# Kernel tuning notes

Hardware: AMD Instinct MI355X
Metric: run time of the kernel (lower is better)

The kernel has to match this reference:

```python
import jax, jax.numpy as jnp
import numpy as np

N_HEADS = 16
EMBED_DIM = 1024
HEAD_DIM = EMBED_DIM // N_HEADS
B, S = 4, 2048


def setup_inputs() -> dict:
    key = jax.random.key(0)
    k1, k2, k3, k4 = jax.random.split(key, 4)
    scale = 1.0 / np.sqrt(EMBED_DIM)
    x = jax.random.normal(k1, (B, S, EMBED_DIM), dtype=jnp.float32)
    Wq = jax.random.normal(k2, (EMBED_DIM, EMBED_DIM), dtype=jnp.float32) * scale
    Wk = jax.random.normal(k3, (EMBED_DIM, EMBED_DIM), dtype=jnp.float32) * scale
    Wv = jax.random.normal(k4, (EMBED_DIM, EMBED_DIM), dtype=jnp.float32) * scale
    return {"x": x, "Wq": Wq, "Wk": Wk, "Wv": Wv}


def reference(x, Wq, Wk, Wv):
    b, s, d = x.shape
    # torch nn.Linear(bias=False): y = x @ W.T
    def proj(W):
        return (x @ W.T).reshape(b, s, N_HEADS, HEAD_DIM).transpose(0, 2, 1, 3)  # [b,h,s,hd]
    q, k, v = proj(Wq), proj(Wk), proj(Wv)
    # scores scaled by sqrt(embed_dim) as in the source (not head_dim)
    scores = jnp.einsum('bhqd,bhkd->bhqk', q, k) / jnp.sqrt(jnp.float32(d))
    attn = jax.nn.softmax(scores, axis=-1)
    out = jnp.einsum('bhqk,bhkd->bhqd', attn, v)  # [b,h,s,hd]
    return out.transpose(0, 2, 1, 3).reshape(b, s, d)
```

## Files before the change

kernel.cpp:

```cpp
#include <hip/hip_runtime.h>

#define S_LEN  2048
#define NHEAD  16
#define HDIM   64
#define DMODEL 1024
#define XN     (4 * 2048 * 1024)
#define WN     (1024 * 1024)

typedef float  floatx4 __attribute__((ext_vector_type(4)));
typedef __bf16 bf16x8  __attribute__((ext_vector_type(8)));
typedef __bf16 bf16x4  __attribute__((ext_vector_type(4)));
typedef unsigned int u32;

union B8 {
  bf16x8 v8;
  bf16x4 v4[2];
  __bf16 e[8];
  uint4  u;
};

typedef __attribute__((address_space(1))) u32 gu32;
typedef __attribute__((address_space(3))) u32 lu32;
__device__ __forceinline__ void gld16(const void* g, void* l) {
  __builtin_amdgcn_global_load_lds((const gu32*)g, (lu32*)l, 16, 0, 0);
}

__global__ __launch_bounds__(256) void cvt_kernel(
    const float* __restrict__ x,  const float* __restrict__ Wq,
    const float* __restrict__ Wk, const float* __restrict__ Wv,
    __bf16* __restrict__ xb, __bf16* __restrict__ Wb)
{
  const size_t base = ((size_t)blockIdx.x * 256 + threadIdx.x) * 8;
  const float* src;
  __bf16* dst;
  float scl = 1.0f;
  if (base < XN) {
    src = x + base;
    dst = xb + base;
  } else {
    const size_t j = base - XN;
    const int mat = (int)(j >> 20);
    const size_t o = j & (WN - 1);
    src = (mat == 0 ? Wq : mat == 1 ? Wk : Wv) + o;
    dst = Wb + ((size_t)mat << 20) + o;
    if (mat == 0) scl = 0.045084220027780106f;
  }
  float4 a = *(const float4*)src;
  float4 b = *(const float4*)(src + 4);
  B8 r;
  r.e[0] = (__bf16)(a.x * scl); r.e[1] = (__bf16)(a.y * scl);
  r.e[2] = (__bf16)(a.z * scl); r.e[3] = (__bf16)(a.w * scl);
  r.e[4] = (__bf16)(b.x * scl); r.e[5] = (__bf16)(b.y * scl);
  r.e[6] = (__bf16)(b.z * scl); r.e[7] = (__bf16)(b.w * scl);
  *(bf16x8*)dst = r.v8;
}

__global__ __launch_bounds__(256) void proj_kernel(
    const __bf16* __restrict__ xb, const __bf16* __restrict__ Wb,
    __bf16* __restrict__ Qo, __bf16* __restrict__ Ko, __bf16* __restrict__ Vt)
{
  __shared__ __attribute__((aligned(16))) union {
    struct { __bf16 As[2][128 * 32]; __bf16 Bs[2][128 * 32]; } st;
    __bf16 Es[4][64][72];
  } sh;

  const int tid  = threadIdx.x;
  const int lane = tid & 63;
  const int wv   = tid >> 6;
  const int l15  = lane & 15;
  const int quad = lane >> 4;

  const int row0 = blockIdx.y * 128;
  const int n0   = blockIdx.x * 128;
  const int wrow = (wv >> 1) * 64;
  const int wcol = (wv & 1) * 64;

  floatx4 acc[4][4];
  #pragma unroll
  for (int i = 0; i < 4; i++)
    #pragma unroll
    for (int j = 0; j < 4; j++) acc[i][j] = (floatx4)0.0f;

  const int swz = quad ^ ((l15 >> 1) & 3);

  const int c0    = tid;
  const int r0_   = c0 >> 2;
  const int g0    = (c0 & 3) ^ ((c0 >> 3) & 3);
  const int c1    = tid + 256;
  const int r1_   = c1 >> 2;
  const int g1    = (c1 & 3) ^ ((c1 >> 3) & 3);
  const size_t l0 = (size_t)(wv * 64) * 8;
  const size_t l1 = (size_t)(wv * 64 + 256) * 8;

  {
    gld16(xb + (size_t)(row0 + r0_) * DMODEL + 0 + g0 * 8, sh.st.As[0] + l0);
    gld16(Wb + (size_t)(n0 + r0_) * DMODEL + 0 + g0 * 8, sh.st.Bs[0] + l0);
    gld16(xb + (size_t)(row0 + r1_) * DMODEL + 0 + g1 * 8, sh.st.As[0] + l1);
    gld16(Wb + (size_t)(n0 + r1_) * DMODEL + 0 + g1 * 8, sh.st.Bs[0] + l1);
  }

  int buf = 0;
  for (int kk = 0; kk < DMODEL; kk += 32) {
    __syncthreads();
    if (kk + 32 < DMODEL) {
      const int nb_ = buf ^ 1;
      const int k2  = kk + 32;
      gld16(xb + (size_t)(row0 + r0_) * DMODEL + k2 + g0 * 8, sh.st.As[nb_] + l0);
      gld16(Wb + (size_t)(n0 + r0_) * DMODEL + k2 + g0 * 8, sh.st.Bs[nb_] + l0);
      gld16(xb + (size_t)(row0 + r1_) * DMODEL + k2 + g1 * 8, sh.st.As[nb_] + l1);
      gld16(Wb + (size_t)(n0 + r1_) * DMODEL + k2 + g1 * 8, sh.st.Bs[nb_] + l1);
    }

    B8 af[4], bg[4];
    #pragma unroll
    for (int mb = 0; mb < 4; mb++)
      af[mb].u = *(const uint4*)(sh.st.As[buf] + (size_t)(wrow + mb * 16 + l15) * 32 + swz * 8);
    #pragma unroll
    for (int nb = 0; nb < 4; nb++)
      bg[nb].u = *(const uint4*)(sh.st.Bs[buf] + (size_t)(wcol + nb * 16 + l15) * 32 + swz * 8);

    #pragma unroll
    for (int mb = 0; mb < 4; mb++)
      #pragma unroll
      for (int nb = 0; nb < 4; nb++)
        acc[mb][nb] = __builtin_amdgcn_mfma_f32_16x16x32_bf16(
            af[mb].v8, bg[nb].v8, acc[mb][nb], 0, 0, 0);
    buf ^= 1;
  }

  const int mat   = n0 >> 10;
  const int bb    = (row0 + wrow) >> 11;
  const int sbase = (row0 + wrow) & 2047;
  const int hh    = ((n0 & 1023) + wcol) >> 6;
  __syncthreads();

  if (mat < 2) {
    #pragma unroll
    for (int mb = 0; mb < 4; mb++)
      #pragma unroll
      for (int rr = 0; rr < 4; rr++)
        #pragma unroll
        for (int nb = 0; nb < 4; nb++)
          sh.Es[wv][mb * 16 + quad * 4 + rr][nb * 16 + l15] =
              (__bf16)acc[mb][nb][rr];
    __bf16* Out = (mat == 0) ? Qo : Ko;
    const size_t obase = ((size_t)(bb * NHEAD + hh) * S_LEN + sbase) * HDIM;
    #pragma unroll
    for (int t = 0; t < 8; t++) {
      const int lin = t * 64 + lane;
      const int s = lin >> 3, g = lin & 7;
      *(uint4*)&Out[obase + (size_t)s * HDIM + g * 8] =
          *(const uint4*)&sh.Es[wv][s][g * 8];
    }
  } else {
    #pragma unroll
    for (int mb = 0; mb < 4; mb++)
      #pragma unroll
      for (int nb = 0; nb < 4; nb++) {
        bf16x4 pk = { (__bf16)acc[mb][nb][0], (__bf16)acc[mb][nb][1],
                      (__bf16)acc[mb][nb][2], (__bf16)acc[mb][nb][3] };
        const int col = 32 * (mb >> 1) + 16 * (quad >> 1) + 8 * (quad & 1) +
                        4 * (mb & 1);
        *(bf16x4*)&sh.Es[wv][nb * 16 + l15][col] = pk;
      }
    const size_t vbase = (size_t)(bb * NHEAD + hh) * HDIM * S_LEN;
    #pragma unroll
    for (int t = 0; t < 8; t++) {
      const int lin = t * 64 + lane;
      const int d = lin >> 3, g = lin & 7;
      *(uint4*)&Vt[vbase + (size_t)d * S_LEN + sbase + g * 8] =
          *(const uint4*)&sh.Es[wv][d][g * 8];
    }
  }
}

__global__ __launch_bounds__(256, 2) void attn_kernel(
    const __bf16* __restrict__ Q, const __bf16* __restrict__ K,
    const __bf16* __restrict__ Vt, float* __restrict__ out)
{
  __shared__ __attribute__((aligned(16))) __bf16 Ks[2][64 * 64];
  __shared__ __attribute__((aligned(16))) __bf16 Vs[2][64 * 64];

  const int tid  = threadIdx.x;
  const int lane = tid & 63;
  const int wv   = tid >> 6;
  const int l15  = lane & 15;
  const int quad = lane >> 4;

  const int bh = blockIdx.x;
  const int q0 = blockIdx.y * 256;
  const int b  = bh >> 4;
  const int h  = bh & 15;

  const __bf16* Qb = Q  + (size_t)bh * S_LEN * HDIM;
  const __bf16* Kb = K  + (size_t)bh * S_LEN * HDIM;
  const __bf16* Vb = Vt + (size_t)bh * HDIM * S_LEN;

  B8 aq[4][2];
  #pragma unroll
  for (int nb = 0; nb < 4; nb++)
    #pragma unroll
    for (int kc = 0; kc < 2; kc++)
      aq[nb][kc].u = *(const uint4*)
          &Qb[(size_t)(q0 + wv * 64 + nb * 16 + l15) * HDIM + kc * 32 + quad * 8];

  floatx4 o[4][4];
  float rs[4];
  #pragma unroll
  for (int mt = 0; mt < 4; mt++)
    #pragma unroll
    for (int nb = 0; nb < 4; nb++) o[mt][nb] = (floatx4)0.0f;
  #pragma unroll
  for (int nb = 0; nb < 4; nb++) rs[nb] = 0.0f;

  const int swz0 = quad ^ (l15 & 7);
  const int swz1 = (4 + quad) ^ (l15 & 7);

  const int rA  = tid >> 3;
  const int gA  = (tid & 7) ^ ((tid >> 3) & 7);
  const int rB  = (tid + 256) >> 3;
  const int gB  = ((tid + 256) & 7) ^ (((tid + 256) >> 3) & 7);
  const size_t lA = (size_t)(wv * 64) * 8;
  const size_t lB = (size_t)(wv * 64 + 256) * 8;

  {
    gld16(Kb + (size_t)rA * HDIM + gA * 8, Ks[0] + lA);
    gld16(Vb + (size_t)rA * S_LEN + gA * 8, Vs[0] + lA);
    gld16(Kb + (size_t)rB * HDIM + gB * 8, Ks[0] + lB);
    gld16(Vb + (size_t)rB * S_LEN + gB * 8, Vs[0] + lB);
  }

  int buf = 0;
  for (int kv0 = 0; kv0 < S_LEN; kv0 += 64) {
    __syncthreads();
    if (kv0 + 64 < S_LEN) {
      const int nbuf = buf ^ 1;
      const int kv1  = kv0 + 64;
      gld16(Kb + (size_t)(kv1 + rA) * HDIM + gA * 8, Ks[nbuf] + lA);
      gld16(Vb + (size_t)rA * S_LEN + kv1 + gA * 8, Vs[nbuf] + lA);
      gld16(Kb + (size_t)(kv1 + rB) * HDIM + gB * 8, Ks[nbuf] + lB);
      gld16(Vb + (size_t)rB * S_LEN + kv1 + gB * 8, Vs[nbuf] + lB);
    }

    floatx4 sa[4][4];
    #pragma unroll
    for (int t = 0; t < 4; t++)
      #pragma unroll
      for (int nb = 0; nb < 4; nb++) sa[t][nb] = (floatx4)0.0f;

    #pragma unroll
    for (int kc = 0; kc < 2; kc++) {
      const int sw = kc ? swz1 : swz0;
      B8 ak[4];
      #pragma unroll
      for (int t = 0; t < 4; t++)
        ak[t].u = *(const uint4*)(Ks[buf] + (size_t)(t * 16 + l15) * 64 + sw * 8);
      #pragma unroll
      for (int t = 0; t < 4; t++)
        #pragma unroll
        for (int nb = 0; nb < 4; nb++)
          sa[t][nb] = __builtin_amdgcn_mfma_f32_16x16x32_bf16(
              ak[t].v8, aq[nb][kc].v8, sa[t][nb], 0, 0, 0);
    }

    #pragma unroll
    for (int kc = 0; kc < 2; kc++) {
      const int sw = kc ? swz1 : swz0;
      B8 pf[4];
      #pragma unroll
      for (int nb = 0; nb < 4; nb++) {
        float e0 = __builtin_amdgcn_exp2f(sa[2 * kc][nb][0]);
        float e1 = __builtin_amdgcn_exp2f(sa[2 * kc][nb][1]);
        float e2 = __builtin_amdgcn_exp2f(sa[2 * kc][nb][2]);
        float e3 = __builtin_amdgcn_exp2f(sa[2 * kc][nb][3]);
        float e4 = __builtin_amdgcn_exp2f(sa[2 * kc + 1][nb][0]);
        float e5 = __builtin_amdgcn_exp2f(sa[2 * kc + 1][nb][1]);
        float e6 = __builtin_amdgcn_exp2f(sa[2 * kc + 1][nb][2]);
        float e7 = __builtin_amdgcn_exp2f(sa[2 * kc + 1][nb][3]);
        rs[nb] += ((e0 + e1) + (e2 + e3)) + ((e4 + e5) + (e6 + e7));
        pf[nb].e[0] = (__bf16)e0; pf[nb].e[1] = (__bf16)e1;
        pf[nb].e[2] = (__bf16)e2; pf[nb].e[3] = (__bf16)e3;
        pf[nb].e[4] = (__bf16)e4; pf[nb].e[5] = (__bf16)e5;
        pf[nb].e[6] = (__bf16)e6; pf[nb].e[7] = (__bf16)e7;
      }
      B8 av[4];
      #pragma unroll
      for (int mt = 0; mt < 4; mt++)
        av[mt].u = *(const uint4*)(Vs[buf] + (size_t)(mt * 16 + l15) * 64 + sw * 8);
      #pragma unroll
      for (int mt = 0; mt < 4; mt++)
        #pragma unroll
        for (int nb = 0; nb < 4; nb++)
          o[mt][nb] = __builtin_amdgcn_mfma_f32_16x16x32_bf16(
              av[mt].v8, pf[nb].v8, o[mt][nb], 0, 0, 0);
    }
    buf ^= 1;
  }

  #pragma unroll
  for (int nb = 0; nb < 4; nb++) {
    float v = rs[nb];
    v += __shfl_xor(v, 16);
    v += __shfl_xor(v, 32);
    const float inv = 1.0f / v;
    const int q = q0 + wv * 64 + nb * 16 + l15;
    #pragma unroll
    for (int mt = 0; mt < 4; mt++) {
      float4 w = { o[mt][nb][0] * inv, o[mt][nb][1] * inv,
                   o[mt][nb][2] * inv, o[mt][nb][3] * inv };
      *(float4*)&out[((size_t)(b * S_LEN + q)) * DMODEL + h * HDIM +
                     mt * 16 + quad * 4] = w;
    }
  }
}

extern "C" void kernel_launch(void* const* d_in, const int* in_sizes, int n_in,
                              void* d_out, int out_size, void* d_ws, size_t ws_size,
                              hipStream_t stream) {
  const float* x  = (const float*)d_in[0];
  const float* Wq = (const float*)d_in[1];
  const float* Wk = (const float*)d_in[2];
  const float* Wv = (const float*)d_in[3];
  float* out = (float*)d_out;

  __bf16* xb = (__bf16*)d_ws;
  __bf16* Wb = xb + XN;
  __bf16* Q  = Wb + 3 * (size_t)WN;
  __bf16* K  = Q + (size_t)XN;
  __bf16* Vt = K + (size_t)XN;

  dim3 b256(256);
  cvt_kernel<<<dim3((XN + 3 * WN) / (256 * 8)), b256, 0, stream>>>(
      x, Wq, Wk, Wv, xb, Wb);

  dim3 g1(24, 64);
  proj_kernel<<<g1, b256, 0, stream>>>(xb, Wb, Q, K, Vt);

  dim3 g2(64, 8);
  attn_kernel<<<g2, b256, 0, stream>>>(Q, K, Vt, out);
}
```

Baseline: 222.9 us.

## Halve attention query tile and drop K/V double buffering for higher occupancy

The attention kernel now gives each block 128 queries instead of 256 (32 per wave), which doubles the grid to 1024 blocks. It also replaces the double-buffered K/V LDS staging with a single buffer loaded at the top of each iteration. Launch bounds are raised to 4 blocks per CU, and the smaller register and LDS footprint is meant to allow more resident waves and better load balance. In exchange, each K/V tile is reused by half as many queries, so global K/V traffic doubles. The load of the next tile no longer overlaps compute, and each iteration adds a second barrier.

```diff
diff --git a/kernel.cpp b/kernel.cpp
--- a/kernel.cpp
+++ b/kernel.cpp
@@ -174,12 +174,12 @@
   }
 }
 
-__global__ __launch_bounds__(256, 2) void attn_kernel(
+__global__ __launch_bounds__(256, 4) void attn_kernel(
     const __bf16* __restrict__ Q, const __bf16* __restrict__ K,
     const __bf16* __restrict__ Vt, float* __restrict__ out)
 {
-  __shared__ __attribute__((aligned(16))) __bf16 Ks[2][64 * 64];
-  __shared__ __attribute__((aligned(16))) __bf16 Vs[2][64 * 64];
+  __shared__ __attribute__((aligned(16))) __bf16 Ks[64 * 64];
+  __shared__ __attribute__((aligned(16))) __bf16 Vs[64 * 64];
 
   const int tid  = threadIdx.x;
   const int lane = tid & 63;
@@ -188,7 +188,7 @@
   const int quad = lane >> 4;
 
   const int bh = blockIdx.x;
-  const int q0 = blockIdx.y * 256;
+  const int q0 = blockIdx.y * 128;
   const int b  = bh >> 4;
   const int h  = bh & 15;
 
@@ -196,22 +196,21 @@
   const __bf16* Kb = K  + (size_t)bh * S_LEN * HDIM;
   const __bf16* Vb = Vt + (size_t)bh * HDIM * S_LEN;
 
-  B8 aq[4][2];
+  B8 aq[2][2];
   #pragma unroll
-  for (int nb = 0; nb < 4; nb++)
+  for (int nb = 0; nb < 2; nb++)
     #pragma unroll
     for (int kc = 0; kc < 2; kc++)
       aq[nb][kc].u = *(const uint4*)
-          &Qb[(size_t)(q0 + wv * 64 + nb * 16 + l15) * HDIM + kc * 32 + quad * 8];
-
-  floatx4 o[4][4];
-  float rs[4];
+          &Qb[(size_t)(q0 + wv * 32 + nb * 16 + l15) * HDIM + kc * 32 + quad * 8];
+
+  floatx4 o[4][2];
+  float rs[2];
   #pragma unroll
   for (int mt = 0; mt < 4; mt++)
     #pragma unroll
-    for (int nb = 0; nb < 4; nb++) o[mt][nb] = (floatx4)0.0f;
-  #pragma unroll
-  for (int nb = 0; nb < 4; nb++) rs[nb] = 0.0f;
+    for (int nb = 0; nb < 2; nb++) o[mt][nb] = (floatx4)0.0f;
+  rs[0] = rs[1] = 0.0f;
 
   const int swz0 = quad ^ (l15 & 7);
   const int swz1 = (4 + quad) ^ (l15 & 7);
@@ -223,30 +222,18 @@
   const size_t lA = (size_t)(wv * 64) * 8;
   const size_t lB = (size_t)(wv * 64 + 256) * 8;
 
-  {
-    gld16(Kb + (size_t)rA * HDIM + gA * 8, Ks[0] + lA);
-    gld16(Vb + (size_t)rA * S_LEN + gA * 8, Vs[0] + lA);
-    gld16(Kb + (size_t)rB * HDIM + gB * 8, Ks[0] + lB);
-    gld16(Vb + (size_t)rB * S_LEN + gB * 8, Vs[0] + lB);
-  }
-
-  int buf = 0;
   for (int kv0 = 0; kv0 < S_LEN; kv0 += 64) {
+    gld16(Kb + (size_t)(kv0 + rA) * HDIM + gA * 8, Ks + lA);
+    gld16(Vb + (size_t)rA * S_LEN + kv0 + gA * 8, Vs + lA);
+    gld16(Kb + (size_t)(kv0 + rB) * HDIM + gB * 8, Ks + lB);
+    gld16(Vb + (size_t)rB * S_LEN + kv0 + gB * 8, Vs + lB);
     __syncthreads();
-    if (kv0 + 64 < S_LEN) {
-      const int nbuf = buf ^ 1;
-      const int kv1  = kv0 + 64;
-      gld16(Kb + (size_t)(kv1 + rA) * HDIM + gA * 8, Ks[nbuf] + lA);
-      gld16(Vb + (size_t)rA * S_LEN + kv1 + gA * 8, Vs[nbuf] + lA);
-      gld16(Kb + (size_t)(kv1 + rB) * HDIM + gB * 8, Ks[nbuf] + lB);
-      gld16(Vb + (size_t)rB * S_LEN + kv1 + gB * 8, Vs[nbuf] + lB);
-    }
-
-    floatx4 sa[4][4];
+
+    floatx4 sa[4][2];
     #pragma unroll
     for (int t = 0; t < 4; t++)
       #pragma unroll
-      for (int nb = 0; nb < 4; nb++) sa[t][nb] = (floatx4)0.0f;
+      for (int nb = 0; nb < 2; nb++) sa[t][nb] = (floatx4)0.0f;
 
     #pragma unroll
     for (int kc = 0; kc < 2; kc++) {
@@ -254,11 +241,11 @@
       B8 ak[4];
       #pragma unroll
       for (int t = 0; t < 4; t++)
-        ak[t].u = *(const uint4*)(Ks[buf] + (size_t)(t * 16 + l15) * 64 + sw * 8);
+        ak[t].u = *(const uint4*)(Ks + (size_t)(t * 16 + l15) * 64 + sw * 8);
       #pragma unroll
       for (int t = 0; t < 4; t++)
         #pragma unroll
-        for (int nb = 0; nb < 4; nb++)
+        for (int nb = 0; nb < 2; nb++)
           sa[t][nb] = __builtin_amdgcn_mfma_f32_16x16x32_bf16(
               ak[t].v8, aq[nb][kc].v8, sa[t][nb], 0, 0, 0);
     }
@@ -266,9 +253,9 @@
     #pragma unroll
     for (int kc = 0; kc < 2; kc++) {
       const int sw = kc ? swz1 : swz0;
-      B8 pf[4];
-      #pragma unroll
-      for (int nb = 0; nb < 4; nb++) {
+      B8 pf[2];
+      #pragma unroll
+      for (int nb = 0; nb < 2; nb++) {
         float e0 = __builtin_amdgcn_exp2f(sa[2 * kc][nb][0]);
         float e1 = __builtin_amdgcn_exp2f(sa[2 * kc][nb][1]);
         float e2 = __builtin_amdgcn_exp2f(sa[2 * kc][nb][2]);
@@ -286,24 +273,24 @@
       B8 av[4];
       #pragma unroll
       for (int mt = 0; mt < 4; mt++)
-        av[mt].u = *(const uint4*)(Vs[buf] + (size_t)(mt * 16 + l15) * 64 + sw * 8);
+        av[mt].u = *(const uint4*)(Vs + (size_t)(mt * 16 + l15) * 64 + sw * 8);
       #pragma unroll
       for (int mt = 0; mt < 4; mt++)
         #pragma unroll
-        for (int nb = 0; nb < 4; nb++)
+        for (int nb = 0; nb < 2; nb++)
           o[mt][nb] = __builtin_amdgcn_mfma_f32_16x16x32_bf16(
               av[mt].v8, pf[nb].v8, o[mt][nb], 0, 0, 0);
     }
-    buf ^= 1;
+    __syncthreads();
   }
 
   #pragma unroll
-  for (int nb = 0; nb < 4; nb++) {
+  for (int nb = 0; nb < 2; nb++) {
     float v = rs[nb];
     v += __shfl_xor(v, 16);
     v += __shfl_xor(v, 32);
     const float inv = 1.0f / v;
-    const int q = q0 + wv * 64 + nb * 16 + l15;
+    const int q = q0 + wv * 32 + nb * 16 + l15;
     #pragma unroll
     for (int mt = 0; mt < 4; mt++) {
       float4 w = { o[mt][nb][0] * inv, o[mt][nb][1] * inv,
@@ -336,6 +323,6 @@
   dim3 g1(24, 64);
   proj_kernel<<<g1, b256, 0, stream>>>(xb, Wb, Q, K, Vt);
 
-  dim3 g2(64, 8);
+  dim3 g2(64, 16);
   attn_kernel<<<g2, b256, 0, stream>>>(Q, K, Vt, out);
 }
```

New measurement: 225.4 us. About the same (+1.1%).
